# Optimization experiments

Hardware: AMD Instinct MI355X
Metric: run time of the kernel (lower is better)

## Reference

```python
import jax, jax.numpy as jnp
import numpy as np

H = 2048          # hidden_size
HK = 16           # linear_num_key_heads
HV = 32           # linear_num_value_heads
DK = 128          # linear_key_head_dim
DV = 128          # linear_value_head_dim
KW = 4            # linear_conv_kernel_dim
KEY_DIM = HK * DK   # 2048
VAL_DIM = HV * DV   # 4096
CONV_DIM = 2 * KEY_DIM + VAL_DIM  # 8192
T = 4096
EPS = 1e-6


def setup_inputs() -> dict:
    key = jax.random.key(0)
    ks = jax.random.split(key, 8)
    w = lambda k, shape, sc=0.02: (jax.random.normal(k, shape, jnp.float32) * sc)
    return {
        "hidden_states": jax.random.normal(ks[0], (T, H), jnp.float32),
        "W_qkvz": w(ks[1], (H, 2 * KEY_DIM + 2 * VAL_DIM)),   # q,k,v,z merged proj
        "W_ba": w(ks[2], (H, 2 * HV)),                        # b,a merged proj
        "conv_w": w(ks[3], (CONV_DIM, KW), 0.1),              # depthwise causal conv
        "A_log": jnp.log(jax.random.uniform(ks[4], (HV,), jnp.float32, 1.0, 16.0)),
        "dt_bias": jnp.ones((HV,), jnp.float32),
        "norm_w": jnp.ones((DV,), jnp.float32),
        "W_out": w(ks[5], (VAL_DIM, H)),
    }


def _l2norm(x):
    return x * jax.lax.rsqrt(jnp.sum(x * x, axis=-1, keepdims=True) + 1e-6)


def reference(hidden_states, W_qkvz, W_ba, conv_w, A_log, dt_bias, norm_w, W_out):
    T_ = hidden_states.shape[0]
    # 1. merged input projections
    qkvz = hidden_states @ W_qkvz                     # [T, 2*key+2*val]
    ba = hidden_states @ W_ba                         # [T, 2*HV]
    q, k, v, z = jnp.split(qkvz, [KEY_DIM, 2 * KEY_DIM, 2 * KEY_DIM + VAL_DIM], axis=-1)
    b, a = jnp.split(ba, 2, axis=-1)

    # 2. short causal depthwise conv1d over q|k|v (z is NOT convolved), then SiLU
    qkv = jnp.concatenate([q, k, v], axis=-1)         # [T, CONV_DIM]
    xp = jnp.pad(qkv, ((KW - 1, 0), (0, 0)))
    y = sum(xp[j:j + T_] * conv_w[:, j] for j in range(KW))
    qkv = jax.nn.silu(y)
    q, k, v = jnp.split(qkv, [KEY_DIM, 2 * KEY_DIM], axis=-1)

    q = _l2norm(q.reshape(T_, HK, DK)) * (DK ** -0.5)
    k = _l2norm(k.reshape(T_, HK, DK))
    v = v.reshape(T_, HV, DV)
    z = z.reshape(T_, HV, DV)

    # GQA-style head expansion
    r = HV // HK
    q = jnp.repeat(q, r, axis=1)                      # [T, HV, DK]
    k = jnp.repeat(k, r, axis=1)

    # gating / delta coefficients
    g = -jnp.exp(A_log) * jax.nn.softplus(a + dt_bias)  # [T, HV] log-decay
    beta = jax.nn.sigmoid(b)                            # [T, HV]

    # 3. gated delta rule recurrence: S_t = exp(g_t)*S + beta_t*k_t(v_t - k_t^T exp(g_t) S)
    def step(S, inp):
        q_t, k_t, v_t, g_t, b_t = inp
        S = S * jnp.exp(g_t)[:, None, None]             # [HV, DK, DV]
        kv = jnp.einsum('hd,hdv->hv', k_t, S)
        delta = (v_t - kv) * b_t[:, None]
        S = S + jnp.einsum('hd,hv->hdv', k_t, delta)
        o_t = jnp.einsum('hd,hdv->hv', q_t, S)
        return S, o_t

    S0 = jnp.zeros((HV, DK, DV), jnp.float32)
    _, o = jax.lax.scan(step, S0, (q, k, v, g, beta))   # o: [T, HV, DV]

    # 4. gated RMSNorm (norm_before_gate=True): rmsnorm(o)*w, then * silu(z)
    var = jnp.mean(o * o, axis=-1, keepdims=True)
    o = o * jax.lax.rsqrt(var + EPS) * norm_w
    o = o * jax.nn.silu(z)

    # 5. output projection
    return o.reshape(T_, VAL_DIM) @ W_out
```

## Files before the change

kernel.cpp:

```cpp
#include <hip/hip_runtime.h>
#include <hip/hip_bf16.h>

#define T_LEN 4096
#define H_DIM 2048
#define HKn 16
#define HVn 32
#define DKn 128
#define DVn 128
#define KEY_DIM 2048
#define VAL_DIM 4096

typedef unsigned int u32;
typedef unsigned short u16;
typedef __attribute__((ext_vector_type(8))) short bf16x8;
typedef __attribute__((ext_vector_type(4))) float f32x4;

__device__ __forceinline__ u16 f2bf(float x){
  u32 u = __float_as_uint(x);
  u32 r = (u + 0x7fffu + ((u>>16)&1u)) >> 16;
  return (u16)r;
}
__device__ __forceinline__ float bf2f(u32 b){ return __uint_as_float(b<<16); }
__device__ __forceinline__ u32 packbf(float a, float b){ return (u32)f2bf(a) | ((u32)f2bf(b)<<16); }

__global__ __launch_bounds__(256) void k_cvt(const float* __restrict__ in, u16* __restrict__ out, int n){
  int i = (blockIdx.x*256 + threadIdx.x)*8;
  if (i >= n) return;
  float4 a = *(const float4*)(in+i);
  float4 b = *(const float4*)(in+i+4);
  uint4 o;
  o.x = packbf(a.x,a.y); o.y = packbf(a.z,a.w);
  o.z = packbf(b.x,b.y); o.w = packbf(b.z,b.w);
  *(uint4*)(out+i) = o;
}

__global__ __launch_bounds__(256) void k_tcvt(const float* __restrict__ in, u16* __restrict__ out, int R, int C){
  __shared__ float tile[32][33];
  int c0 = blockIdx.x*32, r0 = blockIdx.y*32;
  int tx = threadIdx.x & 31, ty = threadIdx.x >> 5;
#pragma unroll
  for (int i=0;i<4;++i) tile[ty+8*i][tx] = in[(size_t)(r0+ty+8*i)*C + c0+tx];
  __syncthreads();
#pragma unroll
  for (int i=0;i<4;++i) out[(size_t)(c0+ty+8*i)*R + r0+tx] = f2bf(tile[tx][ty+8*i]);
}

__global__ __launch_bounds__(256) void k_ba(const float* __restrict__ X, const float* __restrict__ W,
    const float* __restrict__ A_log, const float* __restrict__ dt_bias,
    float* __restrict__ gT, float* __restrict__ bT){
  int tid = threadIdx.x;
  int t = blockIdx.x*4 + (tid>>6);
  int j = tid & 63;
  const float* xr = X + (size_t)t*H_DIM;
  float acc = 0.f;
  for (int k=0;k<H_DIM;k+=4){
    float4 xv = *(const float4*)(xr+k);
    acc += xv.x*W[(size_t)(k+0)*64 + j];
    acc += xv.y*W[(size_t)(k+1)*64 + j];
    acc += xv.z*W[(size_t)(k+2)*64 + j];
    acc += xv.w*W[(size_t)(k+3)*64 + j];
  }
  if (j < HVn) {
    bT[(size_t)j*T_LEN + t] = 1.f/(1.f+__expf(-acc));
  } else {
    int h = j - HVn;
    float x = acc + dt_bias[h];
    float sp = (x > 20.f) ? x : log1pf(__expf(x));
    gT[(size_t)h*T_LEN + t] = -__expf(A_log[h]) * sp;
  }
}

typedef const __attribute__((address_space(1))) u32* gas_t;
typedef __attribute__((address_space(3))) u32* las_t;
__device__ __forceinline__ void gld16(const void* g, void* l){
  __builtin_amdgcn_global_load_lds((gas_t)g, (las_t)l, 16, 0, 0);
}
__device__ __forceinline__ f32x4 mf(bf16x8 a, bf16x8 b, f32x4 c){
  return __builtin_amdgcn_mfma_f32_16x16x32_bf16(a,b,c,0,0,0);
}

#define G2_LDS 131072
#define SWX(a) ((a) ^ ((((a)>>9)&1)<<5))

template<int WRITE_BF16>
__global__ __launch_bounds__(512) void k_g256(const u16* __restrict__ A, const u16* __restrict__ BT,
    void* __restrict__ C1, void* __restrict__ C2, int NS, int M, int N, int K){
  extern __shared__ char sm[];
  const int tid=threadIdx.x, lane=tid&63, wave=tid>>6;
  const int fr=lane&15, fq=lane>>4;
  const int wm=wave>>2, wn=wave&3;
  const int nbm = M>>8, nwg = nbm*(N>>8);
  const int cpx = nwg>>3;
  const int swz = ((int)blockIdx.x & 7)*cpx + ((int)blockIdx.x >> 3);
  const int m0 = (swz % nbm) << 8, n0 = (swz / nbm) << 8;
  const int NK = K >> 5;

  f32x4 acc[8][4];
#pragma unroll
  for (int i=0;i<8;++i)
#pragma unroll
    for (int j=0;j<4;++j) acc[i][j] = (f32x4){0.f,0.f,0.f,0.f};

  auto stageA=[&](int kt){
    char* base = sm + (size_t)(kt&3)*32768;
#pragma unroll
    for (int ld=0; ld<2; ++ld){
      int p = ld*8192 + wave*1024 + lane*16;
      int a = SWX(p);
      gld16((const char*)A + ((size_t)(m0 + (a>>6))*K + kt*32)*2 + (a&63), base + p);
    }
  };
  auto stageB=[&](int kt){
    char* base = sm + (size_t)(kt&3)*32768 + 16384;
#pragma unroll
    for (int ld=0; ld<2; ++ld){
      int p = ld*8192 + wave*1024 + lane*16;
      int a = SWX(p);
      gld16((const char*)BT + ((size_t)(n0 + (a>>6))*K + kt*32)*2 + (a&63), base + p);
    }
  };

  stageA(0); stageB(0); stageA(1); stageB(1); stageA(2); stageB(2);
  __syncthreads();

  for (int kt=0; kt<NK; ++kt){
    const char* bufA = sm + (size_t)(kt&3)*32768;
    const char* bufB = bufA + 16384;
    bf16x8 bfr[4], afr[4];
#pragma unroll
    for (int j=0;j<4;++j){
      int a = (wn*64 + j*16 + fr)*64 + fq*16;
      bfr[j] = *(const bf16x8*)(bufB + SWX(a));
    }
#pragma unroll
    for (int i=0;i<4;++i){
      int a = (wm*128 + i*16 + fr)*64 + fq*16;
      afr[i] = *(const bf16x8*)(bufA + SWX(a));
    }
    if (kt+3 < NK) stageA(kt+3);
    asm volatile("s_barrier" ::: "memory");
    __builtin_amdgcn_s_setprio(1);
#pragma unroll
    for (int i=0;i<4;++i)
#pragma unroll
      for (int j=0;j<4;++j) acc[i][j] = mf(afr[i], bfr[j], acc[i][j]);
    __builtin_amdgcn_s_setprio(0);
    asm volatile("s_barrier" ::: "memory");
#pragma unroll
    for (int i=0;i<4;++i){
      int a = (wm*128 + 64 + i*16 + fr)*64 + fq*16;
      afr[i] = *(const bf16x8*)(bufA + SWX(a));
    }
    if (kt+3 < NK) stageB(kt+3);
    asm volatile("s_barrier" ::: "memory");
    __builtin_amdgcn_s_setprio(1);
#pragma unroll
    for (int i=0;i<4;++i)
#pragma unroll
      for (int j=0;j<4;++j) acc[4+i][j] = mf(afr[i], bfr[j], acc[4+i][j]);
    __builtin_amdgcn_s_setprio(0);
    asm volatile("s_waitcnt vmcnt(8)" ::: "memory");
    asm volatile("s_barrier" ::: "memory");
  }

#pragma unroll
  for (int mt=0; mt<8; ++mt)
#pragma unroll
    for (int nt=0; nt<4; ++nt){
      int row = m0 + wm*128 + mt*16 + fq*4;
      int col = n0 + wn*64 + nt*16 + fr;
#pragma unroll
      for (int r=0;r<4;++r){
        float v = acc[mt][nt][r];
        if (col < NS){
          if (WRITE_BF16) ((u16*)C1)[(size_t)(row+r)*NS + col] = f2bf(v);
          else            ((float*)C1)[(size_t)(row+r)*NS + col] = v;
        } else {
          if (WRITE_BF16) ((u16*)C2)[(size_t)(row+r)*(N-NS) + col-NS] = f2bf(v);
          else            ((float*)C2)[(size_t)(row+r)*(N-NS) + col-NS] = v;
        }
      }
    }
}

#define GW_LDS 98304
__global__ __launch_bounds__(512) void k_gw(const u16* __restrict__ A, const u16* __restrict__ BT,
    float* __restrict__ C, int M, int N, int K){
  extern __shared__ char sm[];
  const int tid=threadIdx.x, lane=tid&63, wave=tid>>6;
  const int fr=lane&15, fq=lane>>4;
  const int wm=wave>>2, wn=wave&3;
  const int nbm=M>>7, nwg=nbm*(N>>8);
  const int cpx=nwg>>3;
  const int swz=((int)blockIdx.x&7)*cpx + ((int)blockIdx.x>>3);
  const int m0=(swz%nbm)<<7, n0=(swz/nbm)<<8;
  const int NK=K>>5;

  f32x4 acc[4][4];
#pragma unroll
  for(int i=0;i<4;++i)
#pragma unroll
    for(int j=0;j<4;++j) acc[i][j]=(f32x4){0.f,0.f,0.f,0.f};

  auto stage=[&](int kt){
    char* base = sm + (size_t)(kt&3)*24576;
    { int p=tid*16; int a=SWX(p);
      gld16((const char*)A + ((size_t)(m0+(a>>6))*K + kt*32)*2 + (a&63), base+p); }
    char* bb = base + 8192;
#pragma unroll
    for(int ld=0;ld<2;++ld){ int p=ld*8192+tid*16; int a=SWX(p);
      gld16((const char*)BT + ((size_t)(n0+(a>>6))*K + kt*32)*2 + (a&63), bb+p); }
  };
  stage(0); stage(1); stage(2);
  __syncthreads();

  for(int kt=0;kt<NK;++kt){
    const char* bufA = sm + (size_t)(kt&3)*24576;
    const char* bufB = bufA + 8192;
    bf16x8 afr[4], bfr[4];
#pragma unroll
    for(int i=0;i<4;++i){ int a=(wm*64+i*16+fr)*64+fq*16; afr[i]=*(const bf16x8*)(bufA+SWX(a)); }
#pragma unroll
    for(int j=0;j<4;++j){ int a=(wn*64+j*16+fr)*64+fq*16; bfr[j]=*(const bf16x8*)(bufB+SWX(a)); }
    if(kt+3<NK) stage(kt+3);
    asm volatile("s_barrier":::"memory");
    __builtin_amdgcn_s_setprio(1);
#pragma unroll
    for(int i=0;i<4;++i)
#pragma unroll
      for(int j=0;j<4;++j) acc[i][j]=mf(afr[i],bfr[j],acc[i][j]);
    __builtin_amdgcn_s_setprio(0);
    asm volatile("s_waitcnt vmcnt(6)":::"memory");
    asm volatile("s_barrier":::"memory");
  }

#pragma unroll
  for(int mt=0;mt<4;++mt)
#pragma unroll
    for(int nt=0;nt<4;++nt){
      int row=m0+wm*64+mt*16+fq*4;
      int col=n0+wn*64+nt*16+fr;
#pragma unroll
      for(int r=0;r<4;++r)
        C[(size_t)(row+r)*N + col] = acc[mt][nt][r];
    }
}

__global__ __launch_bounds__(256) void k_conv(const u16* __restrict__ qkv, const float* __restrict__ cw,
    u16* __restrict__ qn, u16* __restrict__ kn, u16* __restrict__ vv){
  const int r = blockIdx.y;
  const int t0 = blockIdx.x*32;
  const int c = r*2048 + threadIdx.x*8;
  float wgt[8][4];
#pragma unroll
  for(int i=0;i<8;++i){
    float4 wv=*(const float4*)(cw+(size_t)(c+i)*4);
    wgt[i][0]=wv.x;wgt[i][1]=wv.y;wgt[i][2]=wv.z;wgt[i][3]=wv.w;
  }
  float h0[8],h1[8],h2[8];
  if(t0>=3){
    uint4 a=*(const uint4*)(qkv+(size_t)(t0-3)*8192+c);
    uint4 b=*(const uint4*)(qkv+(size_t)(t0-2)*8192+c);
    uint4 d=*(const uint4*)(qkv+(size_t)(t0-1)*8192+c);
    h0[0]=bf2f(a.x&0xffffu);h0[1]=bf2f(a.x>>16);h0[2]=bf2f(a.y&0xffffu);h0[3]=bf2f(a.y>>16);
    h0[4]=bf2f(a.z&0xffffu);h0[5]=bf2f(a.z>>16);h0[6]=bf2f(a.w&0xffffu);h0[7]=bf2f(a.w>>16);
    h1[0]=bf2f(b.x&0xffffu);h1[1]=bf2f(b.x>>16);h1[2]=bf2f(b.y&0xffffu);h1[3]=bf2f(b.y>>16);
    h1[4]=bf2f(b.z&0xffffu);h1[5]=bf2f(b.z>>16);h1[6]=bf2f(b.w&0xffffu);h1[7]=bf2f(b.w>>16);
    h2[0]=bf2f(d.x&0xffffu);h2[1]=bf2f(d.x>>16);h2[2]=bf2f(d.y&0xffffu);h2[3]=bf2f(d.y>>16);
    h2[4]=bf2f(d.z&0xffffu);h2[5]=bf2f(d.z>>16);h2[6]=bf2f(d.w&0xffffu);h2[7]=bf2f(d.w>>16);
  } else {
#pragma unroll
    for(int i=0;i<8;++i){h0[i]=0.f;h1[i]=0.f;h2[i]=0.f;}
  }
  uint4 c0=*(const uint4*)(qkv+(size_t)t0*8192+c);
  uint4 c1=*(const uint4*)(qkv+(size_t)(t0+1)*8192+c);
  uint4 c2=*(const uint4*)(qkv+(size_t)(t0+2)*8192+c);
  for(int it=0; it<32; ++it){
    int t=t0+it;
    uint4 cn = (t+3<T_LEN)? *(const uint4*)(qkv+(size_t)(t+3)*8192+c) : c0;
    float cur[8];
    cur[0]=bf2f(c0.x&0xffffu);cur[1]=bf2f(c0.x>>16);cur[2]=bf2f(c0.y&0xffffu);cur[3]=bf2f(c0.y>>16);
    cur[4]=bf2f(c0.z&0xffffu);cur[5]=bf2f(c0.z>>16);cur[6]=bf2f(c0.w&0xffffu);cur[7]=bf2f(c0.w>>16);
    float y[8];
#pragma unroll
    for(int i=0;i<8;++i)
      y[i]=fmaf(h0[i],wgt[i][0],fmaf(h1[i],wgt[i][1],fmaf(h2[i],wgt[i][2],cur[i]*wgt[i][3])));
#pragma unroll
    for(int i=0;i<8;++i) y[i]=y[i]/(1.f+__expf(-y[i]));
    if(r<=1){
      float ss=0.f;
#pragma unroll
      for(int i=0;i<8;++i) ss+=y[i]*y[i];
      ss+=__shfl_xor(ss,1);ss+=__shfl_xor(ss,2);ss+=__shfl_xor(ss,4);ss+=__shfl_xor(ss,8);
      float sc=1.f/sqrtf(ss+1e-6f);
      if(r==0) sc*=0.08838834764831845f;
#pragma unroll
      for(int i=0;i<8;++i) y[i]*=sc;
      u16* dst=(r==0?qn:kn)+(size_t)t*KEY_DIM+(c-r*2048);
      *(uint4*)dst=make_uint4(packbf(y[0],y[1]),packbf(y[2],y[3]),packbf(y[4],y[5]),packbf(y[6],y[7]));
    } else {
      u16* dst=vv+(size_t)t*VAL_DIM+(c-4096);
      *(uint4*)dst=make_uint4(packbf(y[0],y[1]),packbf(y[2],y[3]),packbf(y[4],y[5]),packbf(y[6],y[7]));
    }
#pragma unroll
    for(int i=0;i<8;++i){h0[i]=h1[i];h1[i]=h2[i];h2[i]=cur[i];}
    c0=c1;c1=c2;c2=cn;
  }
}

#define P1_K    0
#define P1_Q    16384
#define P1_DT   16384
#define P1_WMT  24576
#define P1_KT   32768
#define P1_NBP  49152
#define P1_AQ   57344
#define P1_NBD  65536
#define P1_TII  69632
#define P1_R1T  73728
#define P1_TAB  77824
#define P1_SIZE 78912

#define SW7(r,cb) ((cb) ^ (((r)&7)<<4))
#define SW3(r,cb) ((cb) ^ (((r)&3)<<4))
#define aK(r,cb)   (P1_K   + (r)*256 + SW7(r,cb))
#define aQ2(r,cb)  (P1_Q   + (r)*256 + SW7(r,cb))
#define aKT(d,cb)  (P1_KT  + (d)*128 + SW7(d,cb))
#define aNBP(t,cb) (P1_NBP + (t)*128 + SW7(t,cb))
#define aAQ(t,cb)  (P1_AQ  + (t)*128 + SW7(t,cb))
#define aDT(s,cb)  (P1_DT  + (s)*128 + SW7(s,cb))
#define aWMT(s,cb) (P1_WMT + (s)*128 + SW7(s,cb))
#define aTII(b,r,cb) (P1_TII + (b)*1024 + (r)*64 + SW3(r,cb))
#define aR1T(v,cb)   (P1_R1T + (v)*64 + SW3(v,cb))

__global__ __launch_bounds__(256) void k_prep(const u16* __restrict__ qn, const u16* __restrict__ kn,
    const float* __restrict__ gT, const float* __restrict__ bT,
    u16* __restrict__ aqmg, u16* __restrict__ kwmg, float* __restrict__ tabg){
  extern __shared__ char sm[];
  const int tid=threadIdx.x, lane=tid&63, wave=tid>>6;
  const int fr=lane&15, fq=lane>>4;
  const int b=blockIdx.x, h=b>>6, c=b&63, kh=h>>1;
  const f32x4 z4={0.f,0.f,0.f,0.f};
  for (int off=P1_NBD+tid*16; off<P1_TAB; off+=4096) *(uint4*)(sm+off)=make_uint4(0,0,0,0);
  {
    int srow = wave*4 + (lane>>4);
    int pb = (lane&15)*16;
#pragma unroll
    for (int r=0;r<4;++r){
      int row=r*16+srow;
      int gcb = pb ^ ((row&7)<<4);
      gld16((const char*)kn + ((size_t)((c<<6)+row)*KEY_DIM + kh*DKn)*2 + gcb, sm + P1_K + r*4096 + wave*1024);
      gld16((const char*)qn + ((size_t)((c<<6)+row)*KEY_DIM + kh*DKn)*2 + gcb, sm + P1_Q + r*4096 + wave*1024);
    }
  }
  float* TB=(float*)(sm+P1_TAB);
  if (wave==0){
    int t=lane;
    float gv=gT[(size_t)h*T_LEN+(c<<6)+t];
    float bv=bT[(size_t)h*T_LEN+(c<<6)+t];
    float s=gv;
    for(int o2=1;o2<64;o2<<=1){ float u=__shfl_up(s,o2,64); if(lane>=o2) s+=u; }
    float cgL=__shfl(s,63,64);
    float gam=__expf(s);
    TB[t]=s; TB[64+t]=gam; TB[128+t]=__expf(cgL-s); TB[192+t]=bv;
    float* tg=tabg+(size_t)b*192;
    tg[t]=gam; tg[64+t]=bv;
    if(t==0) tg[128]=__expf(cgL);
  }
  __syncthreads();
#pragma unroll
  for (int dd=0;dd<2;++dd){
    int tp=tid&31, d0=((tid>>5)+dd*8)*8;
    bf16x8 r0=*(const bf16x8*)(sm+aK(2*tp,d0*2));
    bf16x8 r1=*(const bf16x8*)(sm+aK(2*tp+1,d0*2));
#pragma unroll
    for(int j=0;j<8;++j){
      u32 pk=((u32)(u16)r0[j])|((u32)(u16)r1[j]<<16);
      *(u32*)(sm+aKT(d0+j,tp*4))=pk;
    }
  }
  const int ra=(wave>>1)*32, rb=(wave&1)*32;
  f32x4 kq[2][2], qk[2][2];
#pragma unroll
  for(int ta=0;ta<2;++ta)
#pragma unroll
  for(int tb=0;tb<2;++tb){ kq[ta][tb]=z4; qk[ta][tb]=z4; }
#pragma unroll
  for(int kk=0;kk<4;++kk){
    int cb=kk*64+fq*16;
    bf16x8 Ak0=*(const bf16x8*)(sm+aK(ra+fr,cb));
    bf16x8 Ak1=*(const bf16x8*)(sm+aK(ra+16+fr,cb));
    bf16x8 Aq0=*(const bf16x8*)(sm+aQ2(ra+fr,cb));
    bf16x8 Aq1=*(const bf16x8*)(sm+aQ2(ra+16+fr,cb));
    bf16x8 Bk0=*(const bf16x8*)(sm+aK(rb+fr,cb));
    bf16x8 Bk1=*(const bf16x8*)(sm+aK(rb+16+fr,cb));
    if(ra>=rb)      { kq[0][0]=mf(Ak0,Bk0,kq[0][0]); qk[0][0]=mf(Aq0,Bk0,qk[0][0]); }
    if(ra>=rb+16)   { kq[0][1]=mf(Ak0,Bk1,kq[0][1]); qk[0][1]=mf(Aq0,Bk1,qk[0][1]); }
    if(ra+16>=rb)   { kq[1][0]=mf(Ak1,Bk0,kq[1][0]); qk[1][0]=mf(Aq1,Bk0,qk[1][0]); }
    if(ra+16>=rb+16){ kq[1][1]=mf(Ak1,Bk1,kq[1][1]); qk[1][1]=mf(Aq1,Bk1,qk[1][1]); }
  }
  {
    const float* cg=TB; const float* Be=TB+192;
#pragma unroll
    for(int ta=0;ta<2;++ta)
#pragma unroll
    for(int tb=0;tb<2;++tb){
      int tab=ra+16*ta, tbb=rb+16*tb;
#pragma unroll
      for(int p=0;p<4;++p){
        int t=tab+fq*4+p, s2=tbb+fr;
        float e=__expf(cg[t]-cg[s2]);
        float nv=(s2<t)? -Be[t]*kq[ta][tb][p]*e : 0.f;
        *(u16*)(sm+aNBP(t,s2*2)) = (tbb<tab)? f2bf(nv):(u16)0;
        if(tbb==tab) ((float*)(sm+P1_NBD))[(tab>>4)*256+(fq*4+p)*16+fr]=nv;
        float av=(s2<=t)? qk[ta][tb][p]*e : 0.f;
        *(u16*)(sm+aAQ(t,s2*2)) = f2bf(av);
      }
    }
  }
  __syncthreads();
  for (int off=P1_DT+tid*16; off<P1_DT+16384; off+=4096) *(uint4*)(sm+off)=make_uint4(0,0,0,0);
  {
    int r=lane&15;
    const float* nb=(const float*)(sm+P1_NBD)+wave*256+r*16;
    float n[16], t_[16];
#pragma unroll
    for(int j=0;j<16;++j){ n[j]=nb[j]; t_[j]=(j==r)?1.f:0.f; }
#pragma unroll
    for(int s=0;s<15;++s){
      float tsj[16];
#pragma unroll
      for(int j=0;j<16;++j)
        tsj[j]=__int_as_float(__builtin_amdgcn_ds_bpermute(s*4,__float_as_int(t_[j])));
      if(r>s){
#pragma unroll
        for(int j=0;j<16;++j) t_[j]=fmaf(n[s],tsj[j],t_[j]);
      }
    }
    if(lane<16){
      u32 pk[8];
#pragma unroll
      for(int j=0;j<8;++j) pk[j]=packbf(t_[2*j],t_[2*j+1]);
      *(uint4*)(sm+aTII(wave,r,0)) =make_uint4(pk[0],pk[1],pk[2],pk[3]);
      *(uint4*)(sm+aTII(wave,r,16))=make_uint4(pk[4],pk[5],pk[6],pk[7]);
    }
  }
  __syncthreads();
  {
    const float* WV=TB+128;
    int vb=16*wave;
    for(int i=0;i<4;++i){
      f32x4 acc;
#pragma unroll
      for(int p=0;p<4;++p) acc[p]=(vb+fr==16*i+fq*4+p)?1.f:0.f;
      int np=(i+1)>>1;
      for(int jp=0;jp<np;++jp){
        bf16x8 A=*(const bf16x8*)(sm+aNBP(16*i+fr,jp*64+fq*16));
        bf16x8 B=*(const bf16x8*)(sm+aDT(vb+fr,jp*64+fq*16));
        acc=mf(A,B,acc);
      }
      uint2 w1; w1.x=packbf(acc[0],acc[1]); w1.y=packbf(acc[2],acc[3]);
      *(uint2*)(sm+aR1T(vb+fr,fq*8))=w1;
      bf16x8 At=*(const bf16x8*)(sm+aTII(i,fr,fq*16));
      bf16x8 Bt=*(const bf16x8*)(sm+aR1T(vb+fr,fq*16));
      f32x4 dl=mf(At,Bt,z4);
      int s0=16*i+fq*4;
      uint2 wd; wd.x=packbf(dl[0],dl[1]); wd.y=packbf(dl[2],dl[3]);
      *(uint2*)(sm+aDT(vb+fr,s0*2))=wd;
      uint2 ww; ww.x=packbf(dl[0]*WV[s0],dl[1]*WV[s0+1]); ww.y=packbf(dl[2]*WV[s0+2],dl[3]*WV[s0+3]);
      *(uint2*)(sm+aWMT(vb+fr,s0*2))=ww;
    }
  }
  __syncthreads();
  {
    u16* aout = aqmg + (size_t)b*4096;
#pragma unroll
    for(int ts=0;ts<4;++ts){
      f32x4 acc=z4;
#pragma unroll
      for(int jp=0;jp<2;++jp){
        bf16x8 A=*(const bf16x8*)(sm+aAQ(16*wave+fr,jp*64+fq*16));
        bf16x8 B=*(const bf16x8*)(sm+aDT(16*ts+fr,jp*64+fq*16));
        acc=mf(A,B,acc);
      }
#pragma unroll
      for(int p=0;p<4;++p){
        int t=16*wave+fq*4+p, s=16*ts+fr;
        aout[(t*128 + ((s*2)^((t&7)<<4)))>>1]=f2bf(acc[p]);
      }
    }
    u16* kout = kwmg + (size_t)b*8192;
#pragma unroll
    for(int j=0;j<2;++j){
      int dt=wave+4*j;
#pragma unroll
      for(int st=0;st<4;++st){
        f32x4 acc=z4;
#pragma unroll
        for(int jp=0;jp<2;++jp){
          bf16x8 A=*(const bf16x8*)(sm+aKT(16*dt+fr,jp*64+fq*16));
          bf16x8 B=*(const bf16x8*)(sm+aWMT(16*st+fr,jp*64+fq*16));
          acc=mf(A,B,acc);
        }
#pragma unroll
        for(int p=0;p<4;++p){
          int d=16*dt+fq*4+p, s=16*st+fr;
          kout[(d*128 + ((s*2)^((d&7)<<4)))>>1]=f2bf(acc[p]);
        }
      }
    }
  }
}

#define P2_K(b)   ((b)*16384)
#define P2_Q(b)   (32768 + (b)*16384)
#define P2_W(b)   (65536 + (b)*16384)
#define P2_M(b)   (98304 + (b)*8192)
#define P2_TAB(b) (114688 + (b)*1024)
#define P2_ST(b)  (116736 + (b)*4096)
#define P2_R0T    124928
#define P2_SIZE   126976

#define bKx(b,r,cb)  (P2_K(b) + (r)*256 + SW7(r,cb))
#define bQx(b,r,cb)  (P2_Q(b) + (r)*256 + SW7(r,cb))
#define bWx(b,d,cb)  (P2_W(b) + (d)*128 + SW7(d,cb))
#define bMx(b,t,cb)  (P2_M(b) + (t)*128 + SW7(t,cb))
#define bSTx(b,v,cb) (P2_ST(b) + (v)*256 + SW7(v,cb))
#define bRx(v,cb)    (P2_R0T + (v)*128 + SW7(v,cb))

__global__ __launch_bounds__(256) void k_state(const u16* __restrict__ qn, const u16* __restrict__ kn,
    const u16* __restrict__ vv, const u16* __restrict__ aqmg, const u16* __restrict__ kwmg,
    const float* __restrict__ tabg, u16* __restrict__ ob){
  extern __shared__ char sm[];
  const int tid=threadIdx.x, lane=tid&63, wave=tid>>6;
  const int fr=lane&15, fq=lane>>4;
  const int h=blockIdx.x&31, vs=(blockIdx.x>>5)*16, kh=h>>1;
  const f32x4 z4={0.f,0.f,0.f,0.f};
  for(int off=116736+tid*16; off<124928; off+=4096) *(uint4*)(sm+off)=make_uint4(0,0,0,0);

  auto stage=[&](int c,int b){
    int srow=wave*4+(lane>>4);
    int pb2=(lane&15)*16;
#pragma unroll
    for(int r=0;r<4;++r){
      int row=r*16+srow;
      int gcb=pb2^((row&7)<<4);
      gld16((const char*)kn + ((size_t)((c<<6)+row)*KEY_DIM + kh*DKn)*2 + gcb, sm + P2_K(b)+r*4096+wave*1024);
      gld16((const char*)qn + ((size_t)((c<<6)+row)*KEY_DIM + kh*DKn)*2 + gcb, sm + P2_Q(b)+r*4096+wave*1024);
    }
    const char* wsrc=(const char*)kwmg + (size_t)(h*64+c)*16384;
#pragma unroll
    for(int r=0;r<4;++r)
      gld16(wsrc + r*4096 + wave*1024 + lane*16, sm + P2_W(b)+r*4096+wave*1024);
    const char* msrc=(const char*)aqmg + (size_t)(h*64+c)*8192;
#pragma unroll
    for(int r=0;r<2;++r)
      gld16(msrc + r*4096 + wave*1024 + lane*16, sm + P2_M(b)+r*4096+wave*1024);
    if(wave==0)
      gld16((const char*)tabg + (size_t)(h*64+c)*768 + lane*16, sm + P2_TAB(b));
  };
  u16 vl[4];
  auto loadV=[&](int c){
#pragma unroll
    for(int p=0;p<4;++p)
      vl[p]=vv[(size_t)((c<<6)+16*wave+fq*4+p)*VAL_DIM + h*DVn + vs + fr];
  };

  f32x4 S0=z4, S1=z4;
  stage(0,0); loadV(0);
  __syncthreads();

  for(int c=0;c<64;++c){
    int b=c&1;
    const float* TBf=(const float*)(sm+P2_TAB(b));
    f32x4 ks=z4;
#pragma unroll
    for(int kk=0;kk<4;++kk)
      ks=mf(*(const bf16x8*)(sm+bKx(b,16*wave+fr,kk*64+fq*16)),
            *(const bf16x8*)(sm+bSTx(b,fr,kk*64+fq*16)), ks);
    float r0v[4];
#pragma unroll
    for(int p=0;p<4;++p){
      int t=16*wave+fq*4+p;
      r0v[p]=TBf[64+t]*(bf2f(vl[p]) - TBf[t]*ks[p]);
    }
    uint2 rw; rw.x=packbf(r0v[0],r0v[1]); rw.y=packbf(r0v[2],r0v[3]);
    *(uint2*)(sm+bRx(fr,32*wave+8*fq))=rw;
    __syncthreads();
    if(c<63) stage(c+1,b^1);
    f32x4 qs=z4;
#pragma unroll
    for(int kk=0;kk<4;++kk)
      qs=mf(*(const bf16x8*)(sm+bQx(b,16*wave+fr,kk*64+fq*16)),
            *(const bf16x8*)(sm+bSTx(b,fr,kk*64+fq*16)), qs);
#pragma unroll
    for(int p=0;p<4;++p) qs[p]*=TBf[16*wave+fq*4+p];
#pragma unroll
    for(int jp=0;jp<2;++jp)
      qs=mf(*(const bf16x8*)(sm+bMx(b,16*wave+fr,jp*64+fq*16)),
            *(const bf16x8*)(sm+bRx(fr,jp*64+fq*16)), qs);
#pragma unroll
    for(int p=0;p<4;++p)
      ob[(size_t)((c<<6)+16*wave+fq*4+p)*VAL_DIM + h*DVn + vs + fr]=f2bf(qs[p]);
    if(c<63) loadV(c+1);
    float gl=TBf[128];
    S0[0]*=gl;S0[1]*=gl;S0[2]*=gl;S0[3]*=gl;
    S1[0]*=gl;S1[1]*=gl;S1[2]*=gl;S1[3]*=gl;
#pragma unroll
    for(int jp=0;jp<2;++jp){
      bf16x8 Br=*(const bf16x8*)(sm+bRx(fr,jp*64+fq*16));
      S0=mf(*(const bf16x8*)(sm+bWx(b,16*wave+fr,jp*64+fq*16)), Br, S0);
      S1=mf(*(const bf16x8*)(sm+bWx(b,16*(wave+4)+fr,jp*64+fq*16)), Br, S1);
    }
    uint2 s0w; s0w.x=packbf(S0[0],S0[1]); s0w.y=packbf(S0[2],S0[3]);
    *(uint2*)(sm+bSTx(b^1,fr,32*wave+8*fq))=s0w;
    uint2 s1w; s1w.x=packbf(S1[0],S1[1]); s1w.y=packbf(S1[2],S1[3]);
    *(uint2*)(sm+bSTx(b^1,fr,32*(wave+4)+8*fq))=s1w;
    __syncthreads();
  }
}

__global__ __launch_bounds__(256) void k_gnorm(const u16* __restrict__ ob, const u16* __restrict__ zq,
    const float* __restrict__ nw, u16* __restrict__ og){
  int t = blockIdx.x;
  int base = threadIdx.x*16;
  const u16* src = ob + (size_t)t*VAL_DIM + base;
  uint4 a0 = *(const uint4*)src;
  uint4 a1 = *(const uint4*)(src+8);
  u32 xr[8] = {a0.x,a0.y,a0.z,a0.w,a1.x,a1.y,a1.z,a1.w};
  float x[16];
#pragma unroll
  for (int p=0;p<8;++p){ x[2*p]=bf2f(xr[p]&0xffffu); x[2*p+1]=bf2f(xr[p]>>16); }
  float ss=0.f;
#pragma unroll
  for (int i=0;i<16;++i) ss += x[i]*x[i];
  ss += __shfl_xor(ss,1); ss += __shfl_xor(ss,2); ss += __shfl_xor(ss,4);
  float rs = 1.f/sqrtf(ss*(1.f/128.f) + 1e-6f);
  const u16* zp = zq + (size_t)t*VAL_DIM + base;
  uint4 z0 = *(const uint4*)zp;
  uint4 z1 = *(const uint4*)(zp+8);
  u32 zr[8] = {z0.x,z0.y,z0.z,z0.w,z1.x,z1.y,z1.z,z1.w};
  u32 outw[8];
#pragma unroll
  for (int p=0;p<8;++p){
    float za = bf2f(zr[p]&0xffffu), zb = bf2f(zr[p]>>16);
    float sa = za/(1.f+__expf(-za)), sb = zb/(1.f+__expf(-zb));
    int i0 = p*2, i1 = p*2+1;
    float oa = x[i0]*rs*nw[(base+i0)&127]*sa;
    float obv = x[i1]*rs*nw[(base+i1)&127]*sb;
    outw[p] = packbf(oa, obv);
  }
  uint4* dst = (uint4*)(og + (size_t)t*VAL_DIM + base);
  dst[0] = make_uint4(outw[0],outw[1],outw[2],outw[3]);
  dst[1] = make_uint4(outw[4],outw[5],outw[6],outw[7]);
}

extern "C" void kernel_launch(void* const* d_in, const int* in_sizes, int n_in,
                              void* d_out, int out_size, void* d_ws, size_t ws_size,
                              hipStream_t stream) {
  const float* hidden  = (const float*)d_in[0];
  const float* W_qkvz  = (const float*)d_in[1];
  const float* W_ba    = (const float*)d_in[2];
  const float* conv_w  = (const float*)d_in[3];
  const float* A_log   = (const float*)d_in[4];
  const float* dt_bias = (const float*)d_in[5];
  const float* norm_w  = (const float*)d_in[6];
  const float* W_out   = (const float*)d_in[7];

  char* w = (char*)d_ws;
  size_t need = 252706816;
  if (ws_size < need) return;

  u16*   Xb   = (u16*)(w + 0);
  u16*   W1T  = (u16*)(w + 16777216);
  u16*   QKV  = (u16*)(w + 67108864);
  u16*   Z    = (u16*)(w + 134217728);
  u16*   QN   = (u16*)(w + 167772160);
  u16*   KN   = (u16*)(w + 184549376);
  u16*   V    = (u16*)(w + 201326592);
  u16*   WoT  = (u16*)(w + 234881024);
  float* GTb  = (float*)(w + 251658240);
  float* BTb  = (float*)(w + 252182528);
  u16*   OB   = (u16*)(w + 0);
  u16*   AQMg = (u16*)(w + 67108864);
  u16*   KWMg = (u16*)(w + 83886080);
  float* TABg = (float*)(w + 117440512);
  u16*   OG   = (u16*)(w + 167772160);

  static int smem_set = 0;
  if (!smem_set){
    hipFuncSetAttribute((const void*)k_prep,  hipFuncAttributeMaxDynamicSharedMemorySize, P1_SIZE);
    hipFuncSetAttribute((const void*)k_state, hipFuncAttributeMaxDynamicSharedMemorySize, P2_SIZE);
    hipFuncSetAttribute((const void*)k_g256<1>, hipFuncAttributeMaxDynamicSharedMemorySize, G2_LDS);
    hipFuncSetAttribute((const void*)k_gw, hipFuncAttributeMaxDynamicSharedMemorySize, GW_LDS);
    smem_set = 1;
  }

  k_cvt<<<4096,256,0,stream>>>(hidden, Xb, T_LEN*H_DIM);
  k_tcvt<<<dim3(12288/32, H_DIM/32),256,0,stream>>>(W_qkvz, W1T, H_DIM, 12288);
  k_tcvt<<<dim3(H_DIM/32, VAL_DIM/32),256,0,stream>>>(W_out, WoT, VAL_DIM, H_DIM);
  k_ba<<<T_LEN/4,256,0,stream>>>(hidden, W_ba, A_log, dt_bias, GTb, BTb);
  k_g256<1><<<768,512,G2_LDS,stream>>>(Xb, W1T, QKV, Z, 8192, T_LEN, 12288, H_DIM);
  k_conv<<<dim3(128,4),256,0,stream>>>(QKV, conv_w, QN, KN, V);
  k_prep<<<2048,256,P1_SIZE,stream>>>(QN, KN, GTb, BTb, AQMg, KWMg, TABg);
  k_state<<<256,256,P2_SIZE,stream>>>(QN, KN, V, AQMg, KWMg, TABg, OB);
  k_gnorm<<<T_LEN,256,0,stream>>>(OB, Z, norm_w, OG);
  k_gw<<<256,512,GW_LDS,stream>>>(OG, WoT, (float*)d_out, T_LEN, H_DIM, VAL_DIM);
}
```

Measured before the change: 664.5 us.

## Load recurrence operands into registers directly and remove GEMM prefetch branches

```diff
diff --git a/kernel.cpp b/kernel.cpp
--- a/kernel.cpp
+++ b/kernel.cpp
@@ -126,6 +126,7 @@
   for (int kt=0; kt<NK; ++kt){
     const char* bufA = sm + (size_t)(kt&3)*32768;
     const char* bufB = bufA + 16384;
+    const int ksn = (kt+3 < NK) ? kt+3 : kt+3-NK;
     bf16x8 bfr[4], afr[4];
 #pragma unroll
     for (int j=0;j<4;++j){
@@ -137,7 +138,15 @@
       int a = (wm*128 + i*16 + fr)*64 + fq*16;
       afr[i] = *(const bf16x8*)(bufA + SWX(a));
     }
-    if (kt+3 < NK) stageA(kt+3);
+    {
+      char* base = sm + (size_t)((kt+3)&3)*32768;
+#pragma unroll
+      for (int ld=0; ld<2; ++ld){
+        int p = ld*8192 + wave*1024 + lane*16;
+        int a = SWX(p);
+        gld16((const char*)A + ((size_t)(m0 + (a>>6))*K + ksn*32)*2 + (a&63), base + p);
+      }
+    }
     asm volatile("s_barrier" ::: "memory");
     __builtin_amdgcn_s_setprio(1);
 #pragma unroll
@@ -151,7 +160,15 @@
       int a = (wm*128 + 64 + i*16 + fr)*64 + fq*16;
       afr[i] = *(const bf16x8*)(bufA + SWX(a));
     }
-    if (kt+3 < NK) stageB(kt+3);
+    {
+      char* base = sm + (size_t)((kt+3)&3)*32768 + 16384;
+#pragma unroll
+      for (int ld=0; ld<2; ++ld){
+        int p = ld*8192 + wave*1024 + lane*16;
+        int a = SWX(p);
+        gld16((const char*)BT + ((size_t)(n0 + (a>>6))*K + ksn*32)*2 + (a&63), base + p);
+      }
+    }
     asm volatile("s_barrier" ::: "memory");
     __builtin_amdgcn_s_setprio(1);
 #pragma unroll
@@ -163,22 +180,22 @@
     asm volatile("s_barrier" ::: "memory");
   }
 
+  const int inc1 = (n0 < NS);
+  const int ldc = inc1 ? NS : (N - NS);
+  const int nb  = inc1 ? n0 : (n0 - NS);
+  u16*   Cb16 = (u16*)(inc1 ? C1 : C2);
+  float* Cbf  = (float*)(inc1 ? C1 : C2);
 #pragma unroll
   for (int mt=0; mt<8; ++mt)
 #pragma unroll
     for (int nt=0; nt<4; ++nt){
       int row = m0 + wm*128 + mt*16 + fq*4;
-      int col = n0 + wn*64 + nt*16 + fr;
+      int col = nb + wn*64 + nt*16 + fr;
 #pragma unroll
       for (int r=0;r<4;++r){
         float v = acc[mt][nt][r];
-        if (col < NS){
-          if (WRITE_BF16) ((u16*)C1)[(size_t)(row+r)*NS + col] = f2bf(v);
-          else            ((float*)C1)[(size_t)(row+r)*NS + col] = v;
-        } else {
-          if (WRITE_BF16) ((u16*)C2)[(size_t)(row+r)*(N-NS) + col-NS] = f2bf(v);
-          else            ((float*)C2)[(size_t)(row+r)*(N-NS) + col-NS] = v;
-        }
+        if (WRITE_BF16) Cb16[(size_t)(row+r)*ldc + col] = f2bf(v);
+        else            Cbf [(size_t)(row+r)*ldc + col] = v;
       }
     }
 }
@@ -202,8 +219,8 @@
 #pragma unroll
     for(int j=0;j<4;++j) acc[i][j]=(f32x4){0.f,0.f,0.f,0.f};
 
-  auto stage=[&](int kt){
-    char* base = sm + (size_t)(kt&3)*24576;
+  auto stage=[&](int kt, int buf){
+    char* base = sm + (size_t)buf*24576;
     { int p=tid*16; int a=SWX(p);
       gld16((const char*)A + ((size_t)(m0+(a>>6))*K + kt*32)*2 + (a&63), base+p); }
     char* bb = base + 8192;
@@ -211,7 +228,7 @@
     for(int ld=0;ld<2;++ld){ int p=ld*8192+tid*16; int a=SWX(p);
       gld16((const char*)BT + ((size_t)(n0+(a>>6))*K + kt*32)*2 + (a&63), bb+p); }
   };
-  stage(0); stage(1); stage(2);
+  stage(0,0); stage(1,1); stage(2,2);
   __syncthreads();
 
   for(int kt=0;kt<NK;++kt){
@@ -222,7 +239,7 @@
     for(int i=0;i<4;++i){ int a=(wm*64+i*16+fr)*64+fq*16; afr[i]=*(const bf16x8*)(bufA+SWX(a)); }
 #pragma unroll
     for(int j=0;j<4;++j){ int a=(wn*64+j*16+fr)*64+fq*16; bfr[j]=*(const bf16x8*)(bufB+SWX(a)); }
-    if(kt+3<NK) stage(kt+3);
+    { int ksn=(kt+3<NK)?kt+3:kt+3-NK; stage(ksn,(kt+3)&3); }
     asm volatile("s_barrier":::"memory");
     __builtin_amdgcn_s_setprio(1);
 #pragma unroll
@@ -486,7 +503,7 @@
 #pragma unroll
       for(int p=0;p<4;++p){
         int t=16*wave+fq*4+p, s=16*ts+fr;
-        aout[(t*128 + ((s*2)^((t&7)<<4)))>>1]=f2bf(acc[p]);
+        aout[t*64 + s]=f2bf(acc[p]);
       }
     }
     u16* kout = kwmg + (size_t)b*8192;
@@ -505,26 +522,17 @@
 #pragma unroll
         for(int p=0;p<4;++p){
           int d=16*dt+fq*4+p, s=16*st+fr;
-          kout[(d*128 + ((s*2)^((d&7)<<4)))>>1]=f2bf(acc[p]);
+          kout[d*64 + s]=f2bf(acc[p]);
         }
       }
     }
   }
 }
 
-#define P2_K(b)   ((b)*16384)
-#define P2_Q(b)   (32768 + (b)*16384)
-#define P2_W(b)   (65536 + (b)*16384)
-#define P2_M(b)   (98304 + (b)*8192)
-#define P2_TAB(b) (114688 + (b)*1024)
-#define P2_ST(b)  (116736 + (b)*4096)
-#define P2_R0T    124928
-#define P2_SIZE   126976
-
-#define bKx(b,r,cb)  (P2_K(b) + (r)*256 + SW7(r,cb))
-#define bQx(b,r,cb)  (P2_Q(b) + (r)*256 + SW7(r,cb))
-#define bWx(b,d,cb)  (P2_W(b) + (d)*128 + SW7(d,cb))
-#define bMx(b,t,cb)  (P2_M(b) + (t)*128 + SW7(t,cb))
+#define P2_ST(b)  ((b)*4096)
+#define P2_R0T    8192
+#define P2_SIZE   10240
+
 #define bSTx(b,v,cb) (P2_ST(b) + (v)*256 + SW7(v,cb))
 #define bRx(v,cb)    (P2_R0T + (v)*128 + SW7(v,cb))
 
@@ -536,87 +544,93 @@
   const int fr=lane&15, fq=lane>>4;
   const int h=blockIdx.x&31, vs=(blockIdx.x>>5)*16, kh=h>>1;
   const f32x4 z4={0.f,0.f,0.f,0.f};
-  for(int off=116736+tid*16; off<124928; off+=4096) *(uint4*)(sm+off)=make_uint4(0,0,0,0);
-
-  auto stage=[&](int c,int b){
-    int srow=wave*4+(lane>>4);
-    int pb2=(lane&15)*16;
-#pragma unroll
-    for(int r=0;r<4;++r){
-      int row=r*16+srow;
-      int gcb=pb2^((row&7)<<4);
-      gld16((const char*)kn + ((size_t)((c<<6)+row)*KEY_DIM + kh*DKn)*2 + gcb, sm + P2_K(b)+r*4096+wave*1024);
-      gld16((const char*)qn + ((size_t)((c<<6)+row)*KEY_DIM + kh*DKn)*2 + gcb, sm + P2_Q(b)+r*4096+wave*1024);
-    }
-    const char* wsrc=(const char*)kwmg + (size_t)(h*64+c)*16384;
-#pragma unroll
-    for(int r=0;r<4;++r)
-      gld16(wsrc + r*4096 + wave*1024 + lane*16, sm + P2_W(b)+r*4096+wave*1024);
-    const char* msrc=(const char*)aqmg + (size_t)(h*64+c)*8192;
-#pragma unroll
-    for(int r=0;r<2;++r)
-      gld16(msrc + r*4096 + wave*1024 + lane*16, sm + P2_M(b)+r*4096+wave*1024);
-    if(wave==0)
-      gld16((const char*)tabg + (size_t)(h*64+c)*768 + lane*16, sm + P2_TAB(b));
+  for(int off=tid*16; off<P2_SIZE; off+=4096) *(uint4*)(sm+off)=make_uint4(0,0,0,0);
+
+  const int trow = 16*wave + fr;
+  const int t0   = 16*wave + fq*4;
+
+  bf16x8 kC[4],qC[4],wC[4],mC[2], kN[4],qN[4],wN[4],mN[2];
+  float4 gamC,betC,gamN,betN; float glC,glN;
+  u16 vl[4];
+
+  auto loadOps=[&](int c, bf16x8* K4, bf16x8* Q4, bf16x8* W4, bf16x8* M2,
+                   float4& gam, float4& bet, float& gl){
+    const u16* kb = kn + (size_t)((c<<6)+trow)*KEY_DIM + kh*DKn;
+    const u16* qb = qn + (size_t)((c<<6)+trow)*KEY_DIM + kh*DKn;
+#pragma unroll
+    for(int kk=0;kk<4;++kk){
+      K4[kk]=*(const bf16x8*)(kb + kk*32 + fq*8);
+      Q4[kk]=*(const bf16x8*)(qb + kk*32 + fq*8);
+    }
+    const u16* wb = kwmg + (size_t)(h*64+c)*8192;
+    W4[0]=*(const bf16x8*)(wb + trow*64 + fq*8);
+    W4[1]=*(const bf16x8*)(wb + trow*64 + 32 + fq*8);
+    W4[2]=*(const bf16x8*)(wb + (trow+64)*64 + fq*8);
+    W4[3]=*(const bf16x8*)(wb + (trow+64)*64 + 32 + fq*8);
+    const u16* mb = aqmg + (size_t)(h*64+c)*4096;
+    M2[0]=*(const bf16x8*)(mb + trow*64 + fq*8);
+    M2[1]=*(const bf16x8*)(mb + trow*64 + 32 + fq*8);
+    const float* tb = tabg + (size_t)(h*64+c)*192;
+    gam = *(const float4*)(tb + t0);
+    bet = *(const float4*)(tb + 64 + t0);
+    gl  = tb[128];
   };
-  u16 vl[4];
   auto loadV=[&](int c){
 #pragma unroll
     for(int p=0;p<4;++p)
-      vl[p]=vv[(size_t)((c<<6)+16*wave+fq*4+p)*VAL_DIM + h*DVn + vs + fr];
+      vl[p]=vv[(size_t)((c<<6)+t0+p)*VAL_DIM + h*DVn + vs + fr];
   };
 
   f32x4 S0=z4, S1=z4;
-  stage(0,0); loadV(0);
+  loadOps(0,kC,qC,wC,mC,gamC,betC,glC); loadV(0);
   __syncthreads();
 
   for(int c=0;c<64;++c){
     int b=c&1;
-    const float* TBf=(const float*)(sm+P2_TAB(b));
     f32x4 ks=z4;
 #pragma unroll
     for(int kk=0;kk<4;++kk)
-      ks=mf(*(const bf16x8*)(sm+bKx(b,16*wave+fr,kk*64+fq*16)),
-            *(const bf16x8*)(sm+bSTx(b,fr,kk*64+fq*16)), ks);
+      ks=mf(kC[kk], *(const bf16x8*)(sm+bSTx(b,fr,kk*64+fq*16)), ks);
     float r0v[4];
 #pragma unroll
-    for(int p=0;p<4;++p){
-      int t=16*wave+fq*4+p;
-      r0v[p]=TBf[64+t]*(bf2f(vl[p]) - TBf[t]*ks[p]);
-    }
+    for(int p=0;p<4;++p)
+      r0v[p]=betC[p]*(bf2f(vl[p]) - gamC[p]*ks[p]);
     uint2 rw; rw.x=packbf(r0v[0],r0v[1]); rw.y=packbf(r0v[2],r0v[3]);
     *(uint2*)(sm+bRx(fr,32*wave+8*fq))=rw;
     __syncthreads();
-    if(c<63) stage(c+1,b^1);
+    if(c<63) loadOps(c+1,kN,qN,wN,mN,gamN,betN,glN);
     f32x4 qs=z4;
 #pragma unroll
     for(int kk=0;kk<4;++kk)
-      qs=mf(*(const bf16x8*)(sm+bQx(b,16*wave+fr,kk*64+fq*16)),
-            *(const bf16x8*)(sm+bSTx(b,fr,kk*64+fq*16)), qs);
-#pragma unroll
-    for(int p=0;p<4;++p) qs[p]*=TBf[16*wave+fq*4+p];
+      qs=mf(qC[kk], *(const bf16x8*)(sm+bSTx(b,fr,kk*64+fq*16)), qs);
+#pragma unroll
+    for(int p=0;p<4;++p) qs[p]*=gamC[p];
 #pragma unroll
     for(int jp=0;jp<2;++jp)
-      qs=mf(*(const bf16x8*)(sm+bMx(b,16*wave+fr,jp*64+fq*16)),
-            *(const bf16x8*)(sm+bRx(fr,jp*64+fq*16)), qs);
+      qs=mf(mC[jp], *(const bf16x8*)(sm+bRx(fr,jp*64+fq*16)), qs);
 #pragma unroll
     for(int p=0;p<4;++p)
-      ob[(size_t)((c<<6)+16*wave+fq*4+p)*VAL_DIM + h*DVn + vs + fr]=f2bf(qs[p]);
+      ob[(size_t)((c<<6)+t0+p)*VAL_DIM + h*DVn + vs + fr]=f2bf(qs[p]);
     if(c<63) loadV(c+1);
-    float gl=TBf[128];
-    S0[0]*=gl;S0[1]*=gl;S0[2]*=gl;S0[3]*=gl;
-    S1[0]*=gl;S1[1]*=gl;S1[2]*=gl;S1[3]*=gl;
+    S0[0]*=glC;S0[1]*=glC;S0[2]*=glC;S0[3]*=glC;
+    S1[0]*=glC;S1[1]*=glC;S1[2]*=glC;S1[3]*=glC;
 #pragma unroll
     for(int jp=0;jp<2;++jp){
       bf16x8 Br=*(const bf16x8*)(sm+bRx(fr,jp*64+fq*16));
-      S0=mf(*(const bf16x8*)(sm+bWx(b,16*wave+fr,jp*64+fq*16)), Br, S0);
-      S1=mf(*(const bf16x8*)(sm+bWx(b,16*(wave+4)+fr,jp*64+fq*16)), Br, S1);
+      S0=mf(wC[jp],   Br, S0);
+      S1=mf(wC[2+jp], Br, S1);
     }
     uint2 s0w; s0w.x=packbf(S0[0],S0[1]); s0w.y=packbf(S0[2],S0[3]);
     *(uint2*)(sm+bSTx(b^1,fr,32*wave+8*fq))=s0w;
     uint2 s1w; s1w.x=packbf(S1[0],S1[1]); s1w.y=packbf(S1[2],S1[3]);
     *(uint2*)(sm+bSTx(b^1,fr,32*(wave+4)+8*fq))=s1w;
     __syncthreads();
+    if(c<63){
+#pragma unroll
+      for(int i=0;i<4;++i){ kC[i]=kN[i]; qC[i]=qN[i]; wC[i]=wN[i]; }
+      mC[0]=mN[0]; mC[1]=mN[1];
+      gamC=gamN; betC=betN; glC=glN;
+    }
   }
 }
 
```

After: 712.0 us. +7.1%, slower.
